# Optimization experiments

Measured on AMD Instinct MI355X. Metric: run time of the kernel, lower is better.

The kernel has to match this reference:

```python
import jax, jax.numpy as jnp
import numpy as np

HIDDEN = 512
MEM = 512
COMM = 512
N = 8192


def setup_inputs() -> dict:
    key = jax.random.key(0)
    ks = jax.random.split(key, 8)
    in_dim = HIDDEN + MEM
    s = 1.0 / np.sqrt(in_dim)
    return {
        "u": jax.random.normal(ks[0], (N, HIDDEN), dtype=jnp.float32),
        "z": jax.random.normal(ks[1], (N, MEM), dtype=jnp.float32),
        # torch Linear weights have shape (out, in); biases init to 0 per _init_weights
        "Wk": jax.random.normal(ks[2], (COMM, in_dim), dtype=jnp.float32) * s,
        "bk": jnp.zeros((COMM,), dtype=jnp.float32),
        "Wv": jax.random.normal(ks[3], (COMM, in_dim), dtype=jnp.float32) * s,
        "bv": jnp.zeros((COMM,), dtype=jnp.float32),
        "Wq": jax.random.normal(ks[4], (COMM, in_dim), dtype=jnp.float32) * s,
        "bq": jnp.zeros((COMM,), dtype=jnp.float32),
    }


def reference(u, z, Wk, bk, Wv, bv, Wq, bq):
    n = u.shape[0]
    scale = jnp.sqrt(jnp.asarray(Wk.shape[0], dtype=u.dtype))
    s = jnp.concatenate([u, z], axis=-1)              # (N, in_dim)
    keys = s @ Wk.T + bk                              # (N, C)
    values = s @ Wv.T + bv                            # (N, C)
    queries = s @ Wq.T + bq                           # (N, C)
    scores = (queries @ keys.T) / scale               # (N, N)
    eye = jnp.eye(n, dtype=bool)
    scores = jnp.where(eye, -jnp.inf, scores)         # self-mask
    comm_attn = jax.nn.softmax(scores, axis=-1)
    comm_attn = jnp.nan_to_num(comm_attn, nan=0.0)
    m_bar = comm_attn @ values                        # (N, C)
    return (m_bar, comm_attn)
```

## Files before the change

### kernel.cpp

```cpp
#include <hip/hip_runtime.h>
#include <hip/hip_bf16.h>
#include <stdint.h>

#define N_TOK 8192
#define IN_DIM 1024
#define CDIM 512
#define NW 1536

typedef short bf16x8 __attribute__((ext_vector_type(8)));
typedef float f32x4 __attribute__((ext_vector_type(4)));

__device__ __forceinline__ unsigned short f2bf(float f) {
  union { float f; unsigned int u; } x; x.f = f;
  unsigned int u = x.u;
  u += 0x7fffu + ((u >> 16) & 1u);
  return (unsigned short)(u >> 16);
}
__device__ __forceinline__ float bf2f(unsigned short us) {
  union { unsigned int u; float f; } x; x.u = ((unsigned int)us) << 16;
  return x.f;
}

#define GLD16(g, l) __builtin_amdgcn_global_load_lds( \
    (const __attribute__((address_space(1))) void*)(g), \
    (__attribute__((address_space(3))) void*)(l), 16, 0, 0)

__global__ __launch_bounds__(256) void k_convert(
    const float* __restrict__ u, const float* __restrict__ z,
    const float* __restrict__ wk, const float* __restrict__ wv,
    const float* __restrict__ wq,
    ushort* __restrict__ Sb, ushort* __restrict__ Wb) {
  const int S4 = N_TOK * IN_DIM / 4;
  const int W4 = NW * IN_DIM / 4;
  const int total = S4 + W4;
  for (int e = blockIdx.x * blockDim.x + threadIdx.x; e < total;
       e += gridDim.x * blockDim.x) {
    float4 v; ushort* dst;
    if (e < S4) {
      int idx = e << 2; int row = idx >> 10; int col = idx & 1023;
      const float* src = (col < 512) ? (u + row * 512 + col)
                                     : (z + row * 512 + (col - 512));
      v = *(const float4*)src;
      dst = Sb + idx;
    } else {
      int idx = (e - S4) << 2; int row = idx >> 10; int col = idx & 1023;
      const float* base = (row < 512) ? wk : (row < 1024 ? wv : wq);
      v = *(const float4*)(base + (size_t)(row & 511) * 1024 + col);
      dst = Wb + idx;
    }
    ushort4 o;
    o.x = f2bf(v.x); o.y = f2bf(v.y); o.z = f2bf(v.z); o.w = f2bf(v.w);
    *(ushort4*)dst = o;
  }
}

__global__ __launch_bounds__(256) void k_kvq(
    const ushort* __restrict__ Sb, const ushort* __restrict__ Wb,
    const float* __restrict__ bk, const float* __restrict__ bv,
    const float* __restrict__ bq,
    ushort* __restrict__ Kb, ushort* __restrict__ Qb, ushort* __restrict__ VT) {
  __shared__ __align__(16) ushort As[128 * 64];
  __shared__ __align__(16) ushort Bs[128 * 64];
  const int tid = threadIdx.x, lane = tid & 63, w = tid >> 6;
  const int wr = w >> 1, wc = w & 1;
  const int tm = blockIdx.x, tn = blockIdx.y;

  f32x4 acc[4][4];
#pragma unroll
  for (int m = 0; m < 4; m++)
#pragma unroll
    for (int n = 0; n < 4; n++) acc[m][n] = (f32x4){0.f, 0.f, 0.f, 0.f};

  const ushort* ga0 = Sb + (size_t)tm * 128 * IN_DIM;
  const ushort* gb0 = Wb + (size_t)tn * 128 * IN_DIM;

  for (int k0 = 0; k0 < IN_DIM; k0 += 64) {
#pragma unroll
    for (int i = 0; i < 4; i++) {
      int ce = i * 256 + tid;
      int row = ce >> 3, c8 = (ce & 7) << 3;
      GLD16(ga0 + (size_t)row * IN_DIM + k0 + c8, As + ce * 8);
      GLD16(gb0 + (size_t)row * IN_DIM + k0 + c8, Bs + ce * 8);
    }
    __syncthreads();
#pragma unroll
    for (int kb = 0; kb < 2; kb++) {
      bf16x8 af[4], bfr[4];
#pragma unroll
      for (int m = 0; m < 4; m++)
        af[m] = *(const bf16x8*)(As + (wr * 64 + m * 16 + (lane & 15)) * 64 +
                                 kb * 32 + ((lane >> 4) << 3));
#pragma unroll
      for (int n = 0; n < 4; n++)
        bfr[n] = *(const bf16x8*)(Bs + (wc * 64 + n * 16 + (lane & 15)) * 64 +
                                  kb * 32 + ((lane >> 4) << 3));
#pragma unroll
      for (int m = 0; m < 4; m++)
#pragma unroll
        for (int n = 0; n < 4; n++)
          acc[m][n] = __builtin_amdgcn_mfma_f32_16x16x32_bf16(af[m], bfr[n],
                                                              acc[m][n], 0, 0, 0);
    }
    __syncthreads();
  }

  const int region = tn >> 2;
  const int colr = (tn & 3) * 128 + wc * 64;
  const int rbase = tm * 128 + wr * 64;
  const float* bias = (region == 0) ? bk : (region == 1 ? bv : bq);
  if (region == 1) {
#pragma unroll
    for (int m = 0; m < 4; m++) {
      int r0 = rbase + m * 16 + ((lane >> 4) << 2);
#pragma unroll
      for (int n = 0; n < 4; n++) {
        int c = colr + n * 16 + (lane & 15);
        float b = bias[c];
        ushort4 pk;
        pk.x = f2bf(acc[m][n][0] + b);
        pk.y = f2bf(acc[m][n][1] + b);
        pk.z = f2bf(acc[m][n][2] + b);
        pk.w = f2bf(acc[m][n][3] + b);
        *(ushort4*)(VT + (size_t)c * N_TOK + r0) = pk;
      }
    }
  } else {
    ushort* O = (region == 0) ? Kb : Qb;
#pragma unroll
    for (int m = 0; m < 4; m++) {
      int r0 = rbase + m * 16 + ((lane >> 4) << 2);
#pragma unroll
      for (int n = 0; n < 4; n++) {
        int c = colr + n * 16 + (lane & 15);
        float b = bias[c];
#pragma unroll
        for (int rg = 0; rg < 4; rg++)
          O[(size_t)(r0 + rg) * CDIM + c] = f2bf(acc[m][n][rg] + b);
      }
    }
  }
}

__global__ __launch_bounds__(256) void k_scores(
    const ushort* __restrict__ Qb, const ushort* __restrict__ Kb,
    ushort* __restrict__ E, float* __restrict__ rowpart) {
  __shared__ __align__(16) ushort As[128 * 64];
  __shared__ __align__(16) ushort Bs[128 * 64];
  __shared__ float sums[256];
  const int tid = threadIdx.x, lane = tid & 63, w = tid >> 6;
  const int wr = w >> 1, wc = w & 1;
  const int tm = blockIdx.x, tn = blockIdx.y;

  f32x4 acc[4][4];
#pragma unroll
  for (int m = 0; m < 4; m++)
#pragma unroll
    for (int n = 0; n < 4; n++) acc[m][n] = (f32x4){0.f, 0.f, 0.f, 0.f};

  const ushort* ga0 = Qb + (size_t)tm * 128 * CDIM;
  const ushort* gb0 = Kb + (size_t)tn * 128 * CDIM;

  for (int k0 = 0; k0 < CDIM; k0 += 64) {
#pragma unroll
    for (int i = 0; i < 4; i++) {
      int ce = i * 256 + tid;
      int row = ce >> 3, c8 = (ce & 7) << 3;
      GLD16(ga0 + (size_t)row * CDIM + k0 + c8, As + ce * 8);
      GLD16(gb0 + (size_t)row * CDIM + k0 + c8, Bs + ce * 8);
    }
    __syncthreads();
#pragma unroll
    for (int kb = 0; kb < 2; kb++) {
      bf16x8 af[4], bfr[4];
#pragma unroll
      for (int m = 0; m < 4; m++)
        af[m] = *(const bf16x8*)(As + (wr * 64 + m * 16 + (lane & 15)) * 64 +
                                 kb * 32 + ((lane >> 4) << 3));
#pragma unroll
      for (int n = 0; n < 4; n++)
        bfr[n] = *(const bf16x8*)(Bs + (wc * 64 + n * 16 + (lane & 15)) * 64 +
                                  kb * 32 + ((lane >> 4) << 3));
#pragma unroll
      for (int m = 0; m < 4; m++)
#pragma unroll
        for (int n = 0; n < 4; n++)
          acc[m][n] = __builtin_amdgcn_mfma_f32_16x16x32_bf16(af[m], bfr[n],
                                                              acc[m][n], 0, 0, 0);
    }
    __syncthreads();
  }

  const float scale = 0.044194173824159216f;
  float rs[4][4];
#pragma unroll
  for (int m = 0; m < 4; m++)
#pragma unroll
    for (int rg = 0; rg < 4; rg++) rs[m][rg] = 0.f;

#pragma unroll
  for (int m = 0; m < 4; m++) {
    int grow_b = tm * 128 + wr * 64 + m * 16 + ((lane >> 4) << 2);
#pragma unroll
    for (int n = 0; n < 4; n++) {
      int gcol = tn * 128 + wc * 64 + n * 16 + (lane & 15);
#pragma unroll
      for (int rg = 0; rg < 4; rg++) {
        int grow = grow_b + rg;
        float ev = (grow == gcol) ? 0.0f : __expf(acc[m][n][rg] * scale);
        unsigned short evb = f2bf(ev);
        E[(size_t)grow * N_TOK + gcol] = evb;
        rs[m][rg] += bf2f(evb);
      }
    }
  }
#pragma unroll
  for (int m = 0; m < 4; m++)
#pragma unroll
    for (int rg = 0; rg < 4; rg++) {
      float s = rs[m][rg];
      s += __shfl_xor(s, 1);
      s += __shfl_xor(s, 2);
      s += __shfl_xor(s, 4);
      s += __shfl_xor(s, 8);
      rs[m][rg] = s;
    }
  if ((lane & 15) == 0) {
#pragma unroll
    for (int m = 0; m < 4; m++)
#pragma unroll
      for (int rg = 0; rg < 4; rg++)
        sums[wc * 128 + wr * 64 + m * 16 + ((lane >> 4) << 2) + rg] = rs[m][rg];
  }
  __syncthreads();
  if (tid < 128)
    rowpart[(size_t)(tm * 128 + tid) * 64 + tn] = sums[tid] + sums[128 + tid];
}

__global__ __launch_bounds__(256) void k_rcp(const float* __restrict__ rowpart,
                                             float* __restrict__ rcp_l) {
  int row = blockIdx.x * blockDim.x + threadIdx.x;
  if (row < N_TOK) {
    const float4* p = (const float4*)(rowpart + (size_t)row * 64);
    float s = 0.f;
#pragma unroll
    for (int i = 0; i < 16; i++) {
      float4 v = p[i];
      s += v.x + v.y + v.z + v.w;
    }
    rcp_l[row] = 1.0f / s;
  }
}

__global__ __launch_bounds__(256) void k_pv_norm(
    const ushort* __restrict__ E, const ushort* __restrict__ VT,
    const float* __restrict__ rcp_l, float* __restrict__ part0,
    float* __restrict__ part1, float* __restrict__ attn) {
  __shared__ __align__(16) ushort As[128 * 64];
  __shared__ __align__(16) ushort Bs[64 * 64];
  const int tid = threadIdx.x, lane = tid & 63, w = tid >> 6;
  const int wr = w >> 1, wc = w & 1;
  const int tm = blockIdx.x, tn = blockIdx.y, kz = blockIdx.z;
  const int kbase = kz << 12;

  f32x4 acc[4][2];
#pragma unroll
  for (int m = 0; m < 4; m++)
#pragma unroll
    for (int n = 0; n < 2; n++) acc[m][n] = (f32x4){0.f, 0.f, 0.f, 0.f};

  const ushort* ga0 = E + (size_t)tm * 128 * N_TOK;
  const ushort* gb0 = VT + (size_t)tn * 64 * N_TOK;
  const int kw_lo = kbase + (tn << 9);
  const int kw_hi = kw_lo + 512;
  const int sx = lane & 7;

  for (int k0 = kbase; k0 < kbase + 4096; k0 += 64) {
#pragma unroll
    for (int i = 0; i < 4; i++) {
      int ce = i * 256 + tid;
      int row = ce >> 3;
      int c8 = ((ce & 7) ^ (row & 7)) << 3;
      GLD16(ga0 + (size_t)row * N_TOK + k0 + c8, As + ce * 8);
    }
#pragma unroll
    for (int i = 0; i < 2; i++) {
      int ce = i * 256 + tid;
      int row = ce >> 3;
      int c8 = ((ce & 7) ^ (row & 7)) << 3;
      GLD16(gb0 + (size_t)row * N_TOK + k0 + c8, Bs + ce * 8);
    }
    __syncthreads();
#pragma unroll
    for (int kb = 0; kb < 2; kb++) {
      const int chunk = ((kb * 4 + (lane >> 4)) ^ sx) << 3;
      bf16x8 af[4], bfr[2];
#pragma unroll
      for (int m = 0; m < 4; m++)
        af[m] = *(const bf16x8*)(As + (wr * 64 + m * 16 + (lane & 15)) * 64 +
                                 chunk);
#pragma unroll
      for (int n = 0; n < 2; n++)
        bfr[n] = *(const bf16x8*)(Bs + (wc * 32 + n * 16 + (lane & 15)) * 64 +
                                  chunk);
#pragma unroll
      for (int m = 0; m < 4; m++)
#pragma unroll
        for (int n = 0; n < 2; n++)
          acc[m][n] = __builtin_amdgcn_mfma_f32_16x16x32_bf16(af[m], bfr[n],
                                                              acc[m][n], 0, 0, 0);
    }

    if (attn != nullptr && k0 >= kw_lo && k0 < kw_hi) {
#pragma unroll
      for (int p = 0; p < 4; p++) {
        int ce = p * 256 + tid;
        int row = ce >> 3;
        int c8 = (ce & 7) << 3;
        int grow = tm * 128 + row;
        float rl = rcp_l[grow];
        uint4 ev = *(const uint4*)(E + ((size_t)grow << 13) + k0 + c8);
        float4 o0, o1;
        o0.x = bf2f((unsigned short)(ev.x & 0xffffu)) * rl;
        o0.y = bf2f((unsigned short)(ev.x >> 16)) * rl;
        o0.z = bf2f((unsigned short)(ev.y & 0xffffu)) * rl;
        o0.w = bf2f((unsigned short)(ev.y >> 16)) * rl;
        o1.x = bf2f((unsigned short)(ev.z & 0xffffu)) * rl;
        o1.y = bf2f((unsigned short)(ev.z >> 16)) * rl;
        o1.z = bf2f((unsigned short)(ev.w & 0xffffu)) * rl;
        o1.w = bf2f((unsigned short)(ev.w >> 16)) * rl;
        float* op = attn + ((size_t)grow << 13) + k0 + c8;
        *(float4*)op = o0;
        *(float4*)(op + 4) = o1;
      }
    }
    __syncthreads();
  }

  float* P = kz ? part1 : part0;
#pragma unroll
  for (int m = 0; m < 4; m++) {
    int r0 = tm * 128 + wr * 64 + m * 16 + ((lane >> 4) << 2);
#pragma unroll
    for (int n = 0; n < 2; n++) {
      int c = tn * 64 + wc * 32 + n * 16 + (lane & 15);
#pragma unroll
      for (int rg = 0; rg < 4; rg++)
        P[(size_t)(r0 + rg) * CDIM + c] = acc[m][n][rg];
    }
  }
}

__global__ __launch_bounds__(256) void k_reduce_split(
    float* __restrict__ part0, const float* __restrict__ part1,
    const float* __restrict__ rcp_l) {
  int idx4 = blockIdx.x * blockDim.x + threadIdx.x;
  const int T4 = N_TOK * CDIM / 4;
  if (idx4 < T4) {
    int row = idx4 >> 7;
    float rl = rcp_l[row];
    float4 a = ((const float4*)part0)[idx4];
    float4 b = ((const float4*)part1)[idx4];
    float4 o;
    o.x = (a.x + b.x) * rl; o.y = (a.y + b.y) * rl;
    o.z = (a.z + b.z) * rl; o.w = (a.w + b.w) * rl;
    ((float4*)part0)[idx4] = o;
  }
}

__global__ __launch_bounds__(256) void k_norm(
    const ushort* __restrict__ E, float* __restrict__ attn,
    const float* __restrict__ rcp_l, int row0, int nrows) {
  const int units = nrows << 10;
  for (int uidx = blockIdx.x * blockDim.x + threadIdx.x; uidx < units;
       uidx += gridDim.x * blockDim.x) {
    int row = row0 + (uidx >> 10);
    int c8 = (uidx & 1023) << 3;
    const float rl = rcp_l[row];
    uint4 ev = *(const uint4*)(E + ((size_t)row << 13) + c8);
    float4 o0, o1;
    o0.x = bf2f((unsigned short)(ev.x & 0xffffu)) * rl;
    o0.y = bf2f((unsigned short)(ev.x >> 16)) * rl;
    o0.z = bf2f((unsigned short)(ev.y & 0xffffu)) * rl;
    o0.w = bf2f((unsigned short)(ev.y >> 16)) * rl;
    o1.x = bf2f((unsigned short)(ev.z & 0xffffu)) * rl;
    o1.y = bf2f((unsigned short)(ev.z >> 16)) * rl;
    o1.z = bf2f((unsigned short)(ev.w & 0xffffu)) * rl;
    o1.w = bf2f((unsigned short)(ev.w >> 16)) * rl;
    float* op = attn + ((size_t)row << 13) + c8;
    *(float4*)op = o0;
    *(float4*)(op + 4) = o1;
  }
}

__global__ __launch_bounds__(256) void k_lastrow(
    const ushort* __restrict__ E, float* __restrict__ attn,
    const float* __restrict__ rcp_l) {
  const int row = N_TOK - 1;
  const int t = threadIdx.x;
  const float rl = rcp_l[row];
  const uint4* src = (const uint4*)(E + ((size_t)row << 13)) + t * 4;
  uint4 rr[4] = {src[0], src[1], src[2], src[3]};
  __syncthreads();
  float* dst = attn + ((size_t)row << 13) + t * 32;
#pragma unroll
  for (int q = 0; q < 4; q++) {
    float4 o0, o1;
    o0.x = bf2f((unsigned short)(rr[q].x & 0xffffu)) * rl;
    o0.y = bf2f((unsigned short)(rr[q].x >> 16)) * rl;
    o0.z = bf2f((unsigned short)(rr[q].y & 0xffffu)) * rl;
    o0.w = bf2f((unsigned short)(rr[q].y >> 16)) * rl;
    o1.x = bf2f((unsigned short)(rr[q].z & 0xffffu)) * rl;
    o1.y = bf2f((unsigned short)(rr[q].z >> 16)) * rl;
    o1.z = bf2f((unsigned short)(rr[q].w & 0xffffu)) * rl;
    o1.w = bf2f((unsigned short)(rr[q].w >> 16)) * rl;
    *(float4*)(dst + q * 8) = o0;
    *(float4*)(dst + q * 8 + 4) = o1;
  }
}

extern "C" void kernel_launch(void* const* d_in, const int* in_sizes, int n_in,
                              void* d_out, int out_size, void* d_ws,
                              size_t ws_size, hipStream_t stream) {
  const float* u  = (const float*)d_in[0];
  const float* z  = (const float*)d_in[1];
  const float* Wk = (const float*)d_in[2];
  const float* bk = (const float*)d_in[3];
  const float* Wv = (const float*)d_in[4];
  const float* bv = (const float*)d_in[5];
  const float* Wq = (const float*)d_in[6];
  const float* bq = (const float*)d_in[7];

  float* mbar = (float*)d_out;
  float* attn = (float*)d_out + (size_t)N_TOK * CDIM;

  char* ws = (char*)d_ws;
  ushort* Kb      = (ushort*)(ws + 0);
  ushort* Qb      = (ushort*)(ws + 8388608);
  ushort* VT      = (ushort*)(ws + 16777216);
  float*  rcp_l   = (float*)(ws + 25165824);
  float*  rowpart = (float*)(ws + 25198592);
  ushort* Sb      = (ushort*)(ws + 27295744);
  ushort* Wb      = (ushort*)(ws + 44072960);
  float*  part1   = (float*)(ws + 0);
  const size_t E_WS_OFF = 27295744;
  const size_t REQ = E_WS_OFF + 134217728;
  const bool ws_mode = (ws_size >= REQ);
  ushort* E = ws_mode ? (ushort*)(ws + E_WS_OFF)
                      : (ushort*)((char*)attn + 134217728);

  k_convert<<<dim3(2048), dim3(256), 0, stream>>>(u, z, Wk, Wv, Wq, Sb, Wb);
  k_kvq<<<dim3(64, 12), dim3(256), 0, stream>>>(Sb, Wb, bk, bv, bq, Kb, Qb, VT);
  k_scores<<<dim3(64, 64), dim3(256), 0, stream>>>(Qb, Kb, E, rowpart);
  k_rcp<<<dim3(32), dim3(256), 0, stream>>>(rowpart, rcp_l);
  k_pv_norm<<<dim3(64, 8, 2), dim3(256), 0, stream>>>(
      E, VT, rcp_l, mbar, part1, ws_mode ? attn : nullptr);
  k_reduce_split<<<dim3(4096), dim3(256), 0, stream>>>(mbar, part1, rcp_l);

  if (!ws_mode) {
    static const int ph[] = {0, 4096, 6144, 7168, 7680, 7936, 8064, 8128,
                             8160, 8176, 8184, 8188, 8190, 8191};
    for (int p = 0; p + 1 < (int)(sizeof(ph) / sizeof(ph[0])); ++p) {
      int a = ph[p], b = ph[p + 1];
      int units = (b - a) << 10;
      int blocks = (units + 255) / 256;
      if (blocks > 2048) blocks = 2048;
      k_norm<<<dim3(blocks), dim3(256), 0, stream>>>(E, attn, rcp_l, a, b - a);
    }
    k_lastrow<<<dim3(1), dim3(256), 0, stream>>>(E, attn, rcp_l);
  }
}
```

Before: 401.4 us.

## Unfuse attn normalization from PV, double-buffer A tiles, swizzle score blocks

```diff
diff --git a/kernel.cpp b/kernel.cpp
--- a/kernel.cpp
+++ b/kernel.cpp
@@ -149,7 +149,9 @@
   __shared__ float sums[256];
   const int tid = threadIdx.x, lane = tid & 63, w = tid >> 6;
   const int wr = w >> 1, wc = w & 1;
-  const int tm = blockIdx.x, tn = blockIdx.y;
+  const int bid = blockIdx.x;
+  const int swz = (bid & 7) * 512 + (bid >> 3);
+  const int tm = swz & 63, tn = swz >> 6;
 
   f32x4 acc[4][4];
 #pragma unroll
@@ -251,12 +253,11 @@
   }
 }
 
-__global__ __launch_bounds__(256) void k_pv_norm(
+__global__ __launch_bounds__(256, 4) void k_pv(
     const ushort* __restrict__ E, const ushort* __restrict__ VT,
-    const float* __restrict__ rcp_l, float* __restrict__ part0,
-    float* __restrict__ part1, float* __restrict__ attn) {
-  __shared__ __align__(16) ushort As[128 * 64];
-  __shared__ __align__(16) ushort Bs[64 * 64];
+    float* __restrict__ part0, float* __restrict__ part1) {
+  __shared__ __align__(16) ushort As0[128 * 64];
+  __shared__ __align__(16) ushort As1[128 * 64];
   const int tid = threadIdx.x, lane = tid & 63, w = tid >> 6;
   const int wr = w >> 1, wc = w & 1;
   const int tm = blockIdx.x, tn = blockIdx.y, kz = blockIdx.z;
@@ -269,70 +270,65 @@
     for (int n = 0; n < 2; n++) acc[m][n] = (f32x4){0.f, 0.f, 0.f, 0.f};
 
   const ushort* ga0 = E + (size_t)tm * 128 * N_TOK;
-  const ushort* gb0 = VT + (size_t)tn * 64 * N_TOK;
-  const int kw_lo = kbase + (tn << 9);
-  const int kw_hi = kw_lo + 512;
+  const ushort* gb[2];
+#pragma unroll
+  for (int n = 0; n < 2; n++)
+    gb[n] = VT + (size_t)(tn * 64 + wc * 32 + n * 16 + (lane & 15)) * N_TOK +
+            ((lane >> 4) << 3);
   const int sx = lane & 7;
 
-  for (int k0 = kbase; k0 < kbase + 4096; k0 += 64) {
+  auto stageA = [&](int t, ushort* buf) {
 #pragma unroll
     for (int i = 0; i < 4; i++) {
       int ce = i * 256 + tid;
       int row = ce >> 3;
       int c8 = ((ce & 7) ^ (row & 7)) << 3;
-      GLD16(ga0 + (size_t)row * N_TOK + k0 + c8, As + ce * 8);
-    }
-#pragma unroll
-    for (int i = 0; i < 2; i++) {
-      int ce = i * 256 + tid;
-      int row = ce >> 3;
-      int c8 = ((ce & 7) ^ (row & 7)) << 3;
-      GLD16(gb0 + (size_t)row * N_TOK + k0 + c8, Bs + ce * 8);
-    }
-    __syncthreads();
+      GLD16(ga0 + (size_t)row * N_TOK + kbase + t * 64 + c8, buf + ce * 8);
+    }
+  };
+  auto loadB = [&](int t, bf16x8 (&dst)[2][2]) {
+    int k0 = kbase + t * 64;
+#pragma unroll
+    for (int kb = 0; kb < 2; kb++)
+#pragma unroll
+      for (int n = 0; n < 2; n++)
+        dst[kb][n] = *(const bf16x8*)(gb[n] + k0 + kb * 32);
+  };
+  auto compute = [&](const ushort* buf, const bf16x8 (&b)[2][2]) {
 #pragma unroll
     for (int kb = 0; kb < 2; kb++) {
       const int chunk = ((kb * 4 + (lane >> 4)) ^ sx) << 3;
-      bf16x8 af[4], bfr[2];
-#pragma unroll
-      for (int m = 0; m < 4; m++)
-        af[m] = *(const bf16x8*)(As + (wr * 64 + m * 16 + (lane & 15)) * 64 +
+      bf16x8 af[4];
+#pragma unroll
+      for (int m = 0; m < 4; m++)
+        af[m] = *(const bf16x8*)(buf + (wr * 64 + m * 16 + (lane & 15)) * 64 +
                                  chunk);
 #pragma unroll
-      for (int n = 0; n < 2; n++)
-        bfr[n] = *(const bf16x8*)(Bs + (wc * 32 + n * 16 + (lane & 15)) * 64 +
-                                  chunk);
-#pragma unroll
       for (int m = 0; m < 4; m++)
 #pragma unroll
         for (int n = 0; n < 2; n++)
-          acc[m][n] = __builtin_amdgcn_mfma_f32_16x16x32_bf16(af[m], bfr[n],
+          acc[m][n] = __builtin_amdgcn_mfma_f32_16x16x32_bf16(af[m], b[kb][n],
                                                               acc[m][n], 0, 0, 0);
     }
-
-    if (attn != nullptr && k0 >= kw_lo && k0 < kw_hi) {
-#pragma unroll
-      for (int p = 0; p < 4; p++) {
-        int ce = p * 256 + tid;
-        int row = ce >> 3;
-        int c8 = (ce & 7) << 3;
-        int grow = tm * 128 + row;
-        float rl = rcp_l[grow];
-        uint4 ev = *(const uint4*)(E + ((size_t)grow << 13) + k0 + c8);
-        float4 o0, o1;
-        o0.x = bf2f((unsigned short)(ev.x & 0xffffu)) * rl;
-        o0.y = bf2f((unsigned short)(ev.x >> 16)) * rl;
-        o0.z = bf2f((unsigned short)(ev.y & 0xffffu)) * rl;
-        o0.w = bf2f((unsigned short)(ev.y >> 16)) * rl;
-        o1.x = bf2f((unsigned short)(ev.z & 0xffffu)) * rl;
-        o1.y = bf2f((unsigned short)(ev.z >> 16)) * rl;
-        o1.z = bf2f((unsigned short)(ev.w & 0xffffu)) * rl;
-        o1.w = bf2f((unsigned short)(ev.w >> 16)) * rl;
-        float* op = attn + ((size_t)grow << 13) + k0 + c8;
-        *(float4*)op = o0;
-        *(float4*)(op + 4) = o1;
-      }
-    }
+  };
+
+  bf16x8 b0[2][2], b1[2][2];
+  stageA(0, As0);
+  loadB(0, b0);
+  __syncthreads();
+
+#pragma unroll 1
+  for (int tp = 0; tp < 32; ++tp) {
+    const int t0 = tp * 2;
+    stageA(t0 + 1, As1);
+    loadB(t0 + 1, b1);
+    compute(As0, b0);
+    __syncthreads();
+    if (tp < 31) {
+      stageA(t0 + 2, As0);
+      loadB(t0 + 2, b0);
+    }
+    compute(As1, b1);
     __syncthreads();
   }
 
@@ -450,13 +446,14 @@
 
   k_convert<<<dim3(2048), dim3(256), 0, stream>>>(u, z, Wk, Wv, Wq, Sb, Wb);
   k_kvq<<<dim3(64, 12), dim3(256), 0, stream>>>(Sb, Wb, bk, bv, bq, Kb, Qb, VT);
-  k_scores<<<dim3(64, 64), dim3(256), 0, stream>>>(Qb, Kb, E, rowpart);
+  k_scores<<<dim3(4096), dim3(256), 0, stream>>>(Qb, Kb, E, rowpart);
   k_rcp<<<dim3(32), dim3(256), 0, stream>>>(rowpart, rcp_l);
-  k_pv_norm<<<dim3(64, 8, 2), dim3(256), 0, stream>>>(
-      E, VT, rcp_l, mbar, part1, ws_mode ? attn : nullptr);
+  k_pv<<<dim3(64, 8, 2), dim3(256), 0, stream>>>(E, VT, mbar, part1);
   k_reduce_split<<<dim3(4096), dim3(256), 0, stream>>>(mbar, part1, rcp_l);
 
-  if (!ws_mode) {
+  if (ws_mode) {
+    k_norm<<<dim3(2048), dim3(256), 0, stream>>>(E, attn, rcp_l, 0, N_TOK);
+  } else {
     static const int ph[] = {0, 4096, 6144, 7168, 7680, 7936, 8064, 8128,
                              8160, 8176, 8184, 8188, 8190, 8191};
     for (int p = 0; p + 1 < (int)(sizeof(ph) / sizeof(ph[0])); ++p) {
```

Result: slower. 449.0 us (+11.9%).
